# Kernel optimization log

Hardware: AMD Instinct MI355X
Metric: run time of the kernel (lower is better)

## Reference

```python
import jax, jax.numpy as jnp
import numpy as np

B, S, H, NH = 4, 2048, 1024, 16
DK = H // NH

def setup_inputs() -> dict:
    key = jax.random.key(0)
    ks = jax.random.split(key, 8)
    query = jax.random.normal(ks[0], (B, S, H), dtype=jnp.float32)
    key_t = jax.random.normal(ks[1], (B, S, H), dtype=jnp.float32)
    value = jax.random.normal(ks[2], (B, S, H), dtype=jnp.float32)
    mask = jnp.ones((B, S), dtype=jnp.int32)
    # Linear weights (torch convention: y = x @ W.T + b)
    sc = 1.0 / np.sqrt(H)
    Wq = jax.random.uniform(ks[3], (H, H), jnp.float32, -sc, sc)
    Wk = jax.random.uniform(ks[4], (H, H), jnp.float32, -sc, sc)
    Wv = jax.random.uniform(ks[5], (H, H), jnp.float32, -sc, sc)
    Wo = jax.random.uniform(ks[6], (H, H), jnp.float32, -sc, sc)
    bo = jax.random.uniform(ks[7], (H,), jnp.float32, -sc, sc)
    return {"query": query, "key": key_t, "value": value, "mask": mask,
            "Wq": Wq, "Wk": Wk, "Wv": Wv, "Wo": Wo, "bo": bo}

def reference(query, key, value, mask, Wq, Wk, Wv, Wo, bo):
    # project and split heads: (B,S,H) -> (B,NH,S,DK)
    def split_heads(x, W):
        y = x @ W.T
        return y.reshape(B, S, NH, DK).transpose(0, 2, 1, 3)
    q = split_heads(query, Wq)
    k = split_heads(key, Wk)
    v = split_heads(value, Wv)
    scores = jnp.einsum('bhqd,bhkd->bhqk', q, k) / jnp.sqrt(jnp.float32(DK))
    # outer-product padding mask: (B,S)x(B,S) -> (B,1,S,S)
    m = (mask[:, :, None] * mask[:, None, :])[:, None, :, :]
    scores = jnp.where(m == 0, jnp.float32(-1e9), scores)
    p = jax.nn.softmax(scores, axis=-1)  # dropout off (eval mode)
    x = jnp.einsum('bhqk,bhkd->bhqd', p, v)
    x = x.transpose(0, 2, 1, 3).reshape(B, S, H)
    return x @ Wo.T + bo
```

## Files before the change

### kernel.cpp

```cpp
#include <hip/hip_runtime.h>

typedef unsigned short u16;
typedef __bf16 bf16x8 __attribute__((ext_vector_type(8)));
typedef float f32x4 __attribute__((ext_vector_type(4)));

#if __has_builtin(__builtin_amdgcn_exp2f)
#define EXP2(x) __builtin_amdgcn_exp2f(x)
#else
#define EXP2(x) exp2f(x)
#endif

__device__ __forceinline__ u16 f2bf(float f) {
    unsigned u = __float_as_uint(f);
    u += 0x7fffu + ((u >> 16) & 1u);
    return (u16)(u >> 16);
}

__device__ __forceinline__ void gll16(const void* g, void* l) {
    __builtin_amdgcn_global_load_lds(
        (const __attribute__((address_space(1))) void*)g,
        (__attribute__((address_space(3))) void*)l, 16, 0, 0);
}

__device__ __forceinline__ void cvt_body(const float* __restrict__ in,
                                         u16* __restrict__ out, int i) {
    float4 v = reinterpret_cast<const float4*>(in)[i];
    unsigned long long pack =
        (unsigned long long)f2bf(v.x) |
        ((unsigned long long)f2bf(v.y) << 16) |
        ((unsigned long long)f2bf(v.z) << 32) |
        ((unsigned long long)f2bf(v.w) << 48);
    reinterpret_cast<unsigned long long*>(out)[i] = pack;
}

__global__ __launch_bounds__(256) void cvt_all(const float* __restrict__ q,
                                               const float* __restrict__ k,
                                               const float* __restrict__ v,
                                               const float* __restrict__ wq,
                                               const float* __restrict__ wk,
                                               const float* __restrict__ wv,
                                               const float* __restrict__ wo,
                                               u16* __restrict__ oq,
                                               u16* __restrict__ ok,
                                               u16* __restrict__ ov,
                                               u16* __restrict__ owq,
                                               u16* __restrict__ owk,
                                               u16* __restrict__ owv,
                                               u16* __restrict__ owo,
                                               int n4, int nw4) {
    int i = blockIdx.x * 256 + threadIdx.x;
    if (i < n4)          cvt_body(q, oq, i);
    else if (i < 2 * n4) cvt_body(k, ok, i - n4);
    else if (i < 3 * n4) cvt_body(v, ov, i - 2 * n4);
    else {
        int j = i - 3 * n4;
        if (j < nw4)          cvt_body(wq, owq, j);
        else if (j < 2 * nw4) cvt_body(wk, owk, j - nw4);
        else if (j < 3 * nw4) cvt_body(wv, owv, j - 2 * nw4);
        else if (j < 4 * nw4) cvt_body(wo, owo, j - 3 * nw4);
    }
}

template<int MODE>
__global__ __launch_bounds__(256) void gemm_bt(const u16* __restrict__ A,
                                               const u16* __restrict__ B,
                                               void* __restrict__ Cv,
                                               const float* __restrict__ bias) {
    constexpr int K = 1024, N = 1024;
    __shared__ __align__(16) u16 As[128 * 64];
    __shared__ __align__(16) u16 Bs[128 * 64];
    const int tid = threadIdx.x;
    const int wv = tid >> 6, lane = tid & 63, g = lane >> 4, li = lane & 15;
    const int row0 = blockIdx.y << 7, col0 = blockIdx.x << 7;
    const int wm = wv >> 1, wn = wv & 1;

    f32x4 acc[4][4] = {};

    for (int k0 = 0; k0 < K; k0 += 64) {
        __syncthreads();
#pragma unroll
        for (int i = 0; i < 4; i++) {
            const int o   = (wv << 12) + (i << 10) + (lane << 4);
            const int row = o >> 7;
            const int cbg = (o & 127) ^ ((row & 7) << 4);
            gll16(A + (size_t)(row0 + row) * K + k0 + (cbg >> 1),
                  (char*)As + (wv << 12) + (i << 10));
        }
#pragma unroll
        for (int i = 0; i < 4; i++) {
            const int o   = (wv << 12) + (i << 10) + (lane << 4);
            const int row = o >> 7;
            const int cbg = (o & 127) ^ ((row & 7) << 4);
            gll16(B + (size_t)(col0 + row) * K + k0 + (cbg >> 1),
                  (char*)Bs + (wv << 12) + (i << 10));
        }
        __syncthreads();

#pragma unroll
        for (int kk = 0; kk < 2; kk++) {
            bf16x8 af[4], bfr[4];
            const int cb = ((kk << 5) + (g << 3)) << 1;
#pragma unroll
            for (int m = 0; m < 4; m++) {
                const int row = (wm << 6) + (m << 4) + li;
                af[m] = *reinterpret_cast<const bf16x8*>(
                    (const char*)As + (row << 7) + (cb ^ ((row & 7) << 4)));
            }
#pragma unroll
            for (int n = 0; n < 4; n++) {
                const int row = (wn << 6) + (n << 4) + li;
                bfr[n] = *reinterpret_cast<const bf16x8*>(
                    (const char*)Bs + (row << 7) + (cb ^ ((row & 7) << 4)));
            }
#pragma unroll
            for (int m = 0; m < 4; m++)
#pragma unroll
                for (int n = 0; n < 4; n++)
                    acc[m][n] = __builtin_amdgcn_mfma_f32_16x16x32_bf16(
                        af[m], bfr[n], acc[m][n], 0, 0, 0);
        }
    }

    if constexpr (MODE == 0 || MODE == 3) {
        constexpr float SC = (MODE == 3) ? 0.180336880f : 1.0f;
        u16* C = (u16*)Cv;
#pragma unroll
        for (int m = 0; m < 4; m++)
#pragma unroll
            for (int n = 0; n < 4; n++)
#pragma unroll
                for (int r = 0; r < 4; r++) {
                    int row = row0 + (wm << 6) + (m << 4) + (g << 2) + r;
                    int col = col0 + (wn << 6) + (n << 4) + li;
                    C[(size_t)row * N + col] = f2bf(acc[m][n][r] * SC);
                }
    } else if constexpr (MODE == 1) {
        float* C = (float*)Cv;
#pragma unroll
        for (int m = 0; m < 4; m++)
#pragma unroll
            for (int n = 0; n < 4; n++)
#pragma unroll
                for (int r = 0; r < 4; r++) {
                    int row = row0 + (wm << 6) + (m << 4) + (g << 2) + r;
                    int col = col0 + (wn << 6) + (n << 4) + li;
                    C[(size_t)row * N + col] = acc[m][n][r] + bias[col];
                }
    } else {
        u16* C = (u16*)Cv;
#pragma unroll
        for (int m = 0; m < 4; m++)
#pragma unroll
            for (int n = 0; n < 4; n++) {
                int srow = row0 + (wm << 6) + (m << 4) + (g << 2);
                int col  = col0 + (wn << 6) + (n << 4) + li;
                int b = srow >> 11, s = srow & 2047;
                int nh = col >> 6, d = col & 63;
                unsigned long long pack =
                    (unsigned long long)f2bf(acc[m][n][0]) |
                    ((unsigned long long)f2bf(acc[m][n][1]) << 16) |
                    ((unsigned long long)f2bf(acc[m][n][2]) << 32) |
                    ((unsigned long long)f2bf(acc[m][n][3]) << 48);
                *reinterpret_cast<unsigned long long*>(
                    C + ((size_t)((b << 4) + nh) * 64 + d) * 2048 + s) = pack;
            }
    }
}

__global__ __launch_bounds__(512, 4) void attn_fwd(const u16* __restrict__ Q,
                                                   const u16* __restrict__ Kp,
                                                   const u16* __restrict__ Vt,
                                                   const int* __restrict__ mask,
                                                   u16* __restrict__ O) {
    constexpr int S = 2048, H = 1024;
    constexpr int K0OFF = 0, K1OFF = 8192, V0OFF = 16384, V1OFF = 24576;
    __shared__ __align__(16) char lds[32768];
    __shared__ int sm_bad;
    const int tid = threadIdx.x, wv = tid >> 6, lane = tid & 63;
    const int g = lane >> 4, li = lane & 15;
    const int bid = blockIdx.x;
    const int swz = ((bid & 7) << 7) + (bid >> 3);
    const int q0 = (swz & 15) << 7, h = (swz >> 4) & 15, b = swz >> 8;
    const char* Kg = (const char*)(Kp + (size_t)b * S * H + h * 64);
    const char* Vg = (const char*)(Vt + (size_t)(b * 16 + h) * 64 * S);

    auto stageK = [&](int koff, int kv2) {
        const int o   = tid << 4;
        const int row = o >> 7;
        const int cbg = (o & 127) ^ ((row & 7) << 4);
        const int gk  = (((row >> 2) & 3) << 4) + ((row >> 4) << 2) + (row & 3);
        gll16(Kg + (size_t)(kv2 + gk) * 2048 + cbg, lds + koff + (wv << 10));
    };
    auto stageV = [&](int voff, int kv2) {
        const int o   = tid << 4;
        const int row = o >> 7;
        const int cbg = (o & 127) ^ ((row & 7) << 4);
        gll16(Vg + (size_t)row * 4096 + kv2 * 2 + cbg, lds + voff + (wv << 10));
    };

    if (tid == 0) sm_bad = 0;
    stageK(K0OFF, 0);
    stageV(V0OFF, 0);
    stageK(K1OFF, 64);

    bf16x8 qf[2];
    {
        const u16* Qrow = Q + (size_t)(b * S + q0 + (wv << 4) + li) * H + h * 64 + (g << 3);
        qf[0] = *reinterpret_cast<const bf16x8*>(Qrow);
        qf[1] = *reinterpret_cast<const bf16x8*>(Qrow + 32);
    }

    int z = 0;
#pragma unroll
    for (int j = 0; j < 4; j++) z |= (mask[b * S + (tid << 2) + j] == 0);
    __syncthreads();
    if (z) sm_bad = 1;

    int offK[2], offV[2];
#pragma unroll
    for (int kk = 0; kk < 2; kk++) {
        offK[kk] = (li << 7) + (((kk << 6) + (g << 4)) ^ ((li & 7) << 4));
        offV[kk] = (li << 7) + (((g << 5) + (kk << 4)) ^ ((li & 7) << 4));
    }

    f32x4 scE[4] = {}, scO[4] = {};
    auto QK = [&](int koff, f32x4 (&sc)[4]) {
#pragma unroll
        for (int n = 0; n < 4; n++) sc[n] = f32x4{};
        __builtin_amdgcn_s_setprio(1);
#pragma unroll
        for (int kk = 0; kk < 2; kk++)
#pragma unroll
            for (int n = 0; n < 4; n++) {
                bf16x8 kf = *reinterpret_cast<const bf16x8*>(
                    lds + koff + offK[kk] + (n << 11));
                sc[n] = __builtin_amdgcn_mfma_f32_16x16x32_bf16(kf, qf[kk], sc[n], 0, 0, 0);
            }
        __builtin_amdgcn_s_setprio(0);
    };

    QK(K0OFF, scE);
    __syncthreads();
    const bool bad = (sm_bad != 0);
    const int  mq  = bad ? mask[b * S + q0 + (wv << 4) + li] : 1;

    f32x4 o_[4] = {};
    float l_ = 0.f;
    bf16x8 pfE[2], pfO[2];

    auto SM = [&](f32x4 (&sc)[4], bf16x8 (&pf)[2], int kv2) {
        if (bad) {
            const unsigned long long kb = __ballot(mask[b * S + kv2 + lane] != 0);
#pragma unroll
            for (int n = 0; n < 4; n++)
#pragma unroll
                for (int r = 0; r < 4; r++) {
                    const int key = (g << 4) + (n << 2) + r;
                    const bool ok = mq && ((kb >> key) & 1ull);
                    sc[n][r] = ok ? sc[n][r] : -1e9f;
                }
        }
        float rs = 0.f;
#pragma unroll
        for (int n = 0; n < 4; n++)
#pragma unroll
            for (int r = 0; r < 4; r++) {
                const float p = EXP2(sc[n][r]);
                sc[n][r] = p;
                rs += p;
            }
        rs += __shfl_xor(rs, 16);
        rs += __shfl_xor(rs, 32);
        l_ += rs;
#pragma unroll
        for (int j = 0; j < 4; j++) {
            pf[0][j]     = (__bf16)sc[0][j];
            pf[0][4 + j] = (__bf16)sc[1][j];
            pf[1][j]     = (__bf16)sc[2][j];
            pf[1][4 + j] = (__bf16)sc[3][j];
        }
    };

    auto PV = [&](int voff, bf16x8 (&pf)[2]) {
        __builtin_amdgcn_s_setprio(1);
#pragma unroll
        for (int kk = 0; kk < 2; kk++)
#pragma unroll
            for (int n = 0; n < 4; n++) {
                bf16x8 vf = *reinterpret_cast<const bf16x8*>(
                    lds + voff + offV[kk] + (n << 11));
                o_[n] = __builtin_amdgcn_mfma_f32_16x16x32_bf16(pf[kk], vf, o_[n], 0, 0, 0);
            }
        __builtin_amdgcn_s_setprio(0);
    };

    for (int kv = 0; kv < S; kv += 128) {
        stageV(V1OFF, kv + 64);
        QK(K1OFF, scO);
        if (kv + 128 < S) stageK(K0OFF, kv + 128);
        SM(scE, pfE, kv);
        PV(V0OFF, pfE);
        __syncthreads();
        if (kv + 128 < S) {
            stageV(V0OFF, kv + 128);
            QK(K0OFF, scE);
        }
        if (kv + 192 < S) stageK(K1OFF, kv + 192);
        SM(scO, pfO, kv + 64);
        PV(V1OFF, pfO);
        __syncthreads();
    }

    float linv[4];
#pragma unroll
    for (int r = 0; r < 4; r++) {
        const float lr = __shfl(l_, (lane & 48) + (g << 2) + r);
        linv[r] = lr > 0.f ? 1.f / lr : 0.f;
    }
#pragma unroll
    for (int n = 0; n < 4; n++)
#pragma unroll
        for (int r = 0; r < 4; r++) {
            const int row = q0 + (wv << 4) + (g << 2) + r;
            const int col = (h << 6) + (n << 4) + li;
            O[(size_t)(b * S + row) * H + col] = f2bf(o_[n][r] * linv[r]);
        }
}

extern "C" void kernel_launch(void* const* d_in, const int* in_sizes, int n_in,
                              void* d_out, int out_size, void* d_ws, size_t ws_size,
                              hipStream_t stream) {
    (void)in_sizes; (void)n_in; (void)out_size; (void)ws_size;
    const float* q    = (const float*)d_in[0];
    const float* k    = (const float*)d_in[1];
    const float* v    = (const float*)d_in[2];
    const int*   mask = (const int*)d_in[3];
    const float* Wq   = (const float*)d_in[4];
    const float* Wk   = (const float*)d_in[5];
    const float* Wv   = (const float*)d_in[6];
    const float* Wo   = (const float*)d_in[7];
    const float* bo   = (const float*)d_in[8];

    const size_t NEL = 8192ull * 1024ull;
    u16* ws  = (u16*)d_ws;
    u16* r0  = ws;
    u16* r1  = ws + NEL;
    u16* r2  = ws + 2 * NEL;
    u16* wqb = ws + 3 * NEL;
    u16* wkb = wqb + 1024 * 1024;
    u16* wvb = wkb + 1024 * 1024;
    u16* wob = wvb + 1024 * 1024;
    u16* r4  = wob + 1024 * 1024;

    const int n4  = (int)(NEL / 4);
    const int nw4 = 262144;
    const int cvt_blocks = (3 * n4 + 4 * nw4 + 255) / 256;
    cvt_all<<<dim3(cvt_blocks), dim3(256), 0, stream>>>(
        q, k, v, Wq, Wk, Wv, Wo, r0, r1, r2, wqb, wkb, wvb, wob, n4, nw4);

    dim3 gg(8, 64), bb(256);
    gemm_bt<3><<<gg, bb, 0, stream>>>(r0, wqb, r4, nullptr);
    gemm_bt<0><<<gg, bb, 0, stream>>>(r1, wkb, r0, nullptr);
    gemm_bt<2><<<gg, bb, 0, stream>>>(r2, wvb, r1, nullptr);

    attn_fwd<<<dim3(1024), dim3(512), 0, stream>>>(r4, r0, r1, mask, r2);

    gemm_bt<1><<<gg, bb, 0, stream>>>(r2, wob, (float*)d_out, bo);
}
```

Baseline: 213.9 us.

## Batch QKV projections into one launch and compute softmax row sums via MFMA

Merges the three Q/K/V projection GEMMs into a single 3D-grid kernel, provided the workspace is large enough, so that one launch fills the GPU with three times as many blocks. Inside attention, the per-tile row-sum reduction (exp accumulation plus cross-lane shuffles) is replaced by an extra MFMA against a vector of ones, and the QK accumulator is seeded with a zero constant instead of being explicitly cleared. The MFMA row sum rounds P to bf16 before summing, which changes the normalisation slightly, and it adds one matrix op per PV step. Falls back to the old sequential launches when the workspace is too small.

```diff
diff --git a/kernel.cpp b/kernel.cpp
--- a/kernel.cpp
+++ b/kernel.cpp
@@ -61,20 +61,15 @@
     }
 }
 
-template<int MODE>
-__global__ __launch_bounds__(256) void gemm_bt(const u16* __restrict__ A,
-                                               const u16* __restrict__ B,
-                                               void* __restrict__ Cv,
-                                               const float* __restrict__ bias) {
-    constexpr int K = 1024, N = 1024;
-    __shared__ __align__(16) u16 As[128 * 64];
-    __shared__ __align__(16) u16 Bs[128 * 64];
+template<typename ACC>
+__device__ __forceinline__ void gemm_core(const u16* __restrict__ A,
+                                          const u16* __restrict__ B,
+                                          u16* As, u16* Bs,
+                                          int row0, int col0, ACC& acc) {
+    constexpr int K = 1024;
     const int tid = threadIdx.x;
     const int wv = tid >> 6, lane = tid & 63, g = lane >> 4, li = lane & 15;
-    const int row0 = blockIdx.y << 7, col0 = blockIdx.x << 7;
     const int wm = wv >> 1, wn = wv & 1;
-
-    f32x4 acc[4][4] = {};
 
     for (int k0 = 0; k0 < K; k0 += 64) {
         __syncthreads();
@@ -120,10 +115,63 @@
                         af[m], bfr[n], acc[m][n], 0, 0, 0);
         }
     }
+}
+
+__device__ __forceinline__ void epi_bf16(f32x4 (&acc)[4][4], u16* C,
+                                         int row0, int col0, float SC) {
+    const int lane = threadIdx.x & 63, g = lane >> 4, li = lane & 15;
+    const int wv = threadIdx.x >> 6, wm = wv >> 1, wn = wv & 1;
+#pragma unroll
+    for (int m = 0; m < 4; m++)
+#pragma unroll
+        for (int n = 0; n < 4; n++)
+#pragma unroll
+            for (int r = 0; r < 4; r++) {
+                int row = row0 + (wm << 6) + (m << 4) + (g << 2) + r;
+                int col = col0 + (wn << 6) + (n << 4) + li;
+                C[(size_t)row * 1024 + col] = f2bf(acc[m][n][r] * SC);
+            }
+}
+
+__device__ __forceinline__ void epi_vt(f32x4 (&acc)[4][4], u16* C,
+                                       int row0, int col0) {
+    const int lane = threadIdx.x & 63, g = lane >> 4, li = lane & 15;
+    const int wv = threadIdx.x >> 6, wm = wv >> 1, wn = wv & 1;
+#pragma unroll
+    for (int m = 0; m < 4; m++)
+#pragma unroll
+        for (int n = 0; n < 4; n++) {
+            int srow = row0 + (wm << 6) + (m << 4) + (g << 2);
+            int col  = col0 + (wn << 6) + (n << 4) + li;
+            int b = srow >> 11, s = srow & 2047;
+            int nh = col >> 6, d = col & 63;
+            unsigned long long pack =
+                (unsigned long long)f2bf(acc[m][n][0]) |
+                ((unsigned long long)f2bf(acc[m][n][1]) << 16) |
+                ((unsigned long long)f2bf(acc[m][n][2]) << 32) |
+                ((unsigned long long)f2bf(acc[m][n][3]) << 48);
+            *reinterpret_cast<unsigned long long*>(
+                C + ((size_t)((b << 4) + nh) * 64 + d) * 2048 + s) = pack;
+        }
+}
+
+template<int MODE>
+__global__ __launch_bounds__(256) void gemm_bt(const u16* __restrict__ A,
+                                               const u16* __restrict__ B,
+                                               void* __restrict__ Cv,
+                                               const float* __restrict__ bias) {
+    __shared__ __align__(16) u16 As[128 * 64];
+    __shared__ __align__(16) u16 Bs[128 * 64];
+    const int row0 = blockIdx.y << 7, col0 = blockIdx.x << 7;
+    f32x4 acc[4][4] = {};
+    gemm_core(A, B, As, Bs, row0, col0, acc);
 
     if constexpr (MODE == 0 || MODE == 3) {
-        constexpr float SC = (MODE == 3) ? 0.180336880f : 1.0f;
-        u16* C = (u16*)Cv;
+        epi_bf16(acc, (u16*)Cv, row0, col0, MODE == 3 ? 0.180336880f : 1.0f);
+    } else if constexpr (MODE == 1) {
+        float* C = (float*)Cv;
+        const int lane = threadIdx.x & 63, g = lane >> 4, li = lane & 15;
+        const int wv = threadIdx.x >> 6, wm = wv >> 1, wn = wv & 1;
 #pragma unroll
         for (int m = 0; m < 4; m++)
 #pragma unroll
@@ -132,39 +180,33 @@
                 for (int r = 0; r < 4; r++) {
                     int row = row0 + (wm << 6) + (m << 4) + (g << 2) + r;
                     int col = col0 + (wn << 6) + (n << 4) + li;
-                    C[(size_t)row * N + col] = f2bf(acc[m][n][r] * SC);
-                }
-    } else if constexpr (MODE == 1) {
-        float* C = (float*)Cv;
-#pragma unroll
-        for (int m = 0; m < 4; m++)
-#pragma unroll
-            for (int n = 0; n < 4; n++)
-#pragma unroll
-                for (int r = 0; r < 4; r++) {
-                    int row = row0 + (wm << 6) + (m << 4) + (g << 2) + r;
-                    int col = col0 + (wn << 6) + (n << 4) + li;
-                    C[(size_t)row * N + col] = acc[m][n][r] + bias[col];
+                    C[(size_t)row * 1024 + col] = acc[m][n][r] + bias[col];
                 }
     } else {
-        u16* C = (u16*)Cv;
-#pragma unroll
-        for (int m = 0; m < 4; m++)
-#pragma unroll
-            for (int n = 0; n < 4; n++) {
-                int srow = row0 + (wm << 6) + (m << 4) + (g << 2);
-                int col  = col0 + (wn << 6) + (n << 4) + li;
-                int b = srow >> 11, s = srow & 2047;
-                int nh = col >> 6, d = col & 63;
-                unsigned long long pack =
-                    (unsigned long long)f2bf(acc[m][n][0]) |
-                    ((unsigned long long)f2bf(acc[m][n][1]) << 16) |
-                    ((unsigned long long)f2bf(acc[m][n][2]) << 32) |
-                    ((unsigned long long)f2bf(acc[m][n][3]) << 48);
-                *reinterpret_cast<unsigned long long*>(
-                    C + ((size_t)((b << 4) + nh) * 64 + d) * 2048 + s) = pack;
-            }
-    }
+        epi_vt(acc, (u16*)Cv, row0, col0);
+    }
+}
+
+__global__ __launch_bounds__(256) void qkv3(const u16* __restrict__ Aq,
+                                            const u16* __restrict__ Ak,
+                                            const u16* __restrict__ Av,
+                                            const u16* __restrict__ Bq,
+                                            const u16* __restrict__ Bk,
+                                            const u16* __restrict__ Bv,
+                                            u16* __restrict__ Cq,
+                                            u16* __restrict__ Ck,
+                                            u16* __restrict__ Cv) {
+    __shared__ __align__(16) u16 As[128 * 64];
+    __shared__ __align__(16) u16 Bs[128 * 64];
+    const int row0 = blockIdx.y << 7, col0 = blockIdx.x << 7;
+    const int zm = blockIdx.z;
+    const u16* A = zm == 0 ? Aq : zm == 1 ? Ak : Av;
+    const u16* B = zm == 0 ? Bq : zm == 1 ? Bk : Bv;
+    u16*       C = zm == 0 ? Cq : zm == 1 ? Ck : Cv;
+    f32x4 acc[4][4] = {};
+    gemm_core(A, B, As, Bs, row0, col0, acc);
+    if (zm == 2)      epi_vt(acc, C, row0, col0);
+    else              epi_bf16(acc, C, row0, col0, zm == 0 ? 0.180336880f : 1.0f);
 }
 
 __global__ __launch_bounds__(512, 4) void attn_fwd(const u16* __restrict__ Q,
@@ -223,19 +265,26 @@
         offV[kk] = (li << 7) + (((g << 5) + (kk << 4)) ^ ((li & 7) << 4));
     }
 
+    const f32x4 zero4 = {};
+    bf16x8 onesf;
+#pragma unroll
+    for (int j = 0; j < 8; j++) onesf[j] = (__bf16)1.0f;
+
     f32x4 scE[4] = {}, scO[4] = {};
     auto QK = [&](int koff, f32x4 (&sc)[4]) {
-#pragma unroll
-        for (int n = 0; n < 4; n++) sc[n] = f32x4{};
         __builtin_amdgcn_s_setprio(1);
 #pragma unroll
-        for (int kk = 0; kk < 2; kk++)
-#pragma unroll
-            for (int n = 0; n < 4; n++) {
-                bf16x8 kf = *reinterpret_cast<const bf16x8*>(
-                    lds + koff + offK[kk] + (n << 11));
-                sc[n] = __builtin_amdgcn_mfma_f32_16x16x32_bf16(kf, qf[kk], sc[n], 0, 0, 0);
-            }
+        for (int n = 0; n < 4; n++) {
+            bf16x8 kf = *reinterpret_cast<const bf16x8*>(
+                lds + koff + offK[0] + (n << 11));
+            sc[n] = __builtin_amdgcn_mfma_f32_16x16x32_bf16(kf, qf[0], zero4, 0, 0, 0);
+        }
+#pragma unroll
+        for (int n = 0; n < 4; n++) {
+            bf16x8 kf = *reinterpret_cast<const bf16x8*>(
+                lds + koff + offK[1] + (n << 11));
+            sc[n] = __builtin_amdgcn_mfma_f32_16x16x32_bf16(kf, qf[1], sc[n], 0, 0, 0);
+        }
         __builtin_amdgcn_s_setprio(0);
     };
 
@@ -245,7 +294,7 @@
     const int  mq  = bad ? mask[b * S + q0 + (wv << 4) + li] : 1;
 
     f32x4 o_[4] = {};
-    float l_ = 0.f;
+    f32x4 o_l = {};
     bf16x8 pfE[2], pfO[2];
 
     auto SM = [&](f32x4 (&sc)[4], bf16x8 (&pf)[2], int kv2) {
@@ -260,18 +309,11 @@
                     sc[n][r] = ok ? sc[n][r] : -1e9f;
                 }
         }
-        float rs = 0.f;
 #pragma unroll
         for (int n = 0; n < 4; n++)
 #pragma unroll
-            for (int r = 0; r < 4; r++) {
-                const float p = EXP2(sc[n][r]);
-                sc[n][r] = p;
-                rs += p;
-            }
-        rs += __shfl_xor(rs, 16);
-        rs += __shfl_xor(rs, 32);
-        l_ += rs;
+            for (int r = 0; r < 4; r++)
+                sc[n][r] = EXP2(sc[n][r]);
 #pragma unroll
         for (int j = 0; j < 4; j++) {
             pf[0][j]     = (__bf16)sc[0][j];
@@ -284,13 +326,15 @@
     auto PV = [&](int voff, bf16x8 (&pf)[2]) {
         __builtin_amdgcn_s_setprio(1);
 #pragma unroll
-        for (int kk = 0; kk < 2; kk++)
+        for (int kk = 0; kk < 2; kk++) {
 #pragma unroll
             for (int n = 0; n < 4; n++) {
                 bf16x8 vf = *reinterpret_cast<const bf16x8*>(
                     lds + voff + offV[kk] + (n << 11));
                 o_[n] = __builtin_amdgcn_mfma_f32_16x16x32_bf16(pf[kk], vf, o_[n], 0, 0, 0);
             }
+            o_l = __builtin_amdgcn_mfma_f32_16x16x32_bf16(pf[kk], onesf, o_l, 0, 0, 0);
+        }
         __builtin_amdgcn_s_setprio(0);
     };
 
@@ -313,10 +357,8 @@
 
     float linv[4];
 #pragma unroll
-    for (int r = 0; r < 4; r++) {
-        const float lr = __shfl(l_, (lane & 48) + (g << 2) + r);
-        linv[r] = lr > 0.f ? 1.f / lr : 0.f;
-    }
+    for (int r = 0; r < 4; r++)
+        linv[r] = o_l[r] > 0.f ? 1.f / o_l[r] : 0.f;
 #pragma unroll
     for (int n = 0; n < 4; n++)
 #pragma unroll
@@ -330,7 +372,7 @@
 extern "C" void kernel_launch(void* const* d_in, const int* in_sizes, int n_in,
                               void* d_out, int out_size, void* d_ws, size_t ws_size,
                               hipStream_t stream) {
-    (void)in_sizes; (void)n_in; (void)out_size; (void)ws_size;
+    (void)in_sizes; (void)n_in; (void)out_size;
     const float* q    = (const float*)d_in[0];
     const float* k    = (const float*)d_in[1];
     const float* v    = (const float*)d_in[2];
@@ -342,28 +384,40 @@
     const float* bo   = (const float*)d_in[8];
 
     const size_t NEL = 8192ull * 1024ull;
+    const size_t WEL = 1024ull * 1024ull;
     u16* ws  = (u16*)d_ws;
-    u16* r0  = ws;
-    u16* r1  = ws + NEL;
-    u16* r2  = ws + 2 * NEL;
+    u16* qb  = ws;
+    u16* kb  = ws + NEL;
+    u16* vb  = ws + 2 * NEL;
     u16* wqb = ws + 3 * NEL;
-    u16* wkb = wqb + 1024 * 1024;
-    u16* wvb = wkb + 1024 * 1024;
-    u16* wob = wvb + 1024 * 1024;
-    u16* r4  = wob + 1024 * 1024;
+    u16* wkb = wqb + WEL;
+    u16* wvb = wkb + WEL;
+    u16* wob = wvb + WEL;
+    u16* p0  = wob + WEL;
 
     const int n4  = (int)(NEL / 4);
-    const int nw4 = 262144;
+    const int nw4 = (int)(WEL / 4);
     const int cvt_blocks = (3 * n4 + 4 * nw4 + 255) / 256;
     cvt_all<<<dim3(cvt_blocks), dim3(256), 0, stream>>>(
-        q, k, v, Wq, Wk, Wv, Wo, r0, r1, r2, wqb, wkb, wvb, wob, n4, nw4);
+        q, k, v, Wq, Wk, Wv, Wo, qb, kb, vb, wqb, wkb, wvb, wob, n4, nw4);
 
     dim3 gg(8, 64), bb(256);
-    gemm_bt<3><<<gg, bb, 0, stream>>>(r0, wqb, r4, nullptr);
-    gemm_bt<0><<<gg, bb, 0, stream>>>(r1, wkb, r0, nullptr);
-    gemm_bt<2><<<gg, bb, 0, stream>>>(r2, wvb, r1, nullptr);
-
-    attn_fwd<<<dim3(1024), dim3(512), 0, stream>>>(r4, r0, r1, mask, r2);
-
-    gemm_bt<1><<<gg, bb, 0, stream>>>(r2, wob, (float*)d_out, bo);
-}
+    const bool fused = ws_size >= (6 * NEL + 4 * WEL) * sizeof(u16);
+
+    if (fused) {
+        u16* Qp = p0;
+        u16* Kp = p0 + NEL;
+        u16* Vt = p0 + 2 * NEL;
+        qkv3<<<dim3(8, 64, 3), bb, 0, stream>>>(qb, kb, vb, wqb, wkb, wvb,
+                                                Qp, Kp, Vt);
+        attn_fwd<<<dim3(1024), dim3(512), 0, stream>>>(Qp, Kp, Vt, mask, qb);
+        gemm_bt<1><<<gg, bb, 0, stream>>>(qb, wob, (float*)d_out, bo);
+    } else {
+        u16* Qp = p0;
+        gemm_bt<3><<<gg, bb, 0, stream>>>(qb, wqb, Qp, nullptr);
+        gemm_bt<0><<<gg, bb, 0, stream>>>(kb, wkb, qb, nullptr);
+        gemm_bt<2><<<gg, bb, 0, stream>>>(vb, wvb, kb, nullptr);
+        attn_fwd<<<dim3(1024), dim3(512), 0, stream>>>(Qp, qb, kb, mask, vb);
+        gemm_bt<1><<<gg, bb, 0, stream>>>(vb, wob, (float*)d_out, bo);
+    }
+}
```

After: 210.8 us. No clear change (-1.4%).
